# Performance work log

Measured on AMD Instinct MI355X. Metric: run time of the kernel, lower is better.

The kernel has to match this reference:

```python
import jax, jax.numpy as jnp
import numpy as np

_SQRT4PI = float(np.sqrt(4.0 * np.pi))

def spherical_harmonics_l2(vec):
    # e3nn real spherical harmonics, lmax=2, normalize=True, normalization='integral'
    # component-normalized values divided by sqrt(4*pi); e3nn (x,y,z) ordering with y as zenith
    r = jnp.linalg.norm(vec, axis=-1, keepdims=True)
    u = vec / jnp.maximum(r, 1e-12)
    x, y, z = u[..., 0], u[..., 1], u[..., 2]
    c1 = np.float32(np.sqrt(3.0)); c2 = np.float32(np.sqrt(15.0)); c3 = np.float32(np.sqrt(5.0))
    sh = jnp.stack([
        jnp.ones_like(x),                      # l=0
        c1 * x, c1 * y, c1 * z,                # l=1
        c2 * x * z,                            # l=2
        c2 * x * y,
        c3 * (y * y - 0.5 * (x * x + z * z)),
        c2 * y * z,
        (c2 * 0.5) * (z * z - x * x),
    ], axis=-1)
    return sh * np.float32(1.0 / _SQRT4PI)

def setup_inputs() -> dict:
    key = jax.random.key(0)
    ks = jax.random.split(key, 8)
    N, M, C, F, SH = 50000, 12, 128, 64, 9
    return dict(
        atom_fea=jax.random.normal(ks[0], (N, C), jnp.float32),
        nbr_fea=jax.random.normal(ks[1], (N, M, F), jnp.float32),
        nbr_idx=jax.random.randint(ks[2], (N, M), 0, N),
        pos=jax.random.normal(ks[3], (N, 3), jnp.float32),
        w1=jax.random.normal(ks[4], (F, F), jnp.float32) * np.float32(1.0 / np.sqrt(F)),
        b1=jnp.zeros((F,), jnp.float32),
        w2=jax.random.normal(ks[5], (F, SH), jnp.float32) * np.float32(1.0 / np.sqrt(F)),
        b2=jnp.zeros((SH,), jnp.float32),
        tp_w=jax.random.normal(ks[6], (C, C), jnp.float32),  # FCTP weight, path (Cx0e)x(1x0e)->(Cx0e)
        bn_gamma=jnp.ones((C,), jnp.float32),
        bn_beta=jnp.zeros((C,), jnp.float32),
    )

def reference(atom_fea, nbr_fea, nbr_idx, pos, w1, b1, w2, b2, tp_w, bn_gamma, bn_beta):
    N, M, F = nbr_fea.shape
    C = atom_fea.shape[1]
    src = nbr_idx.reshape(-1)                                  # (E,)
    h_j = atom_fea[src]                                        # (E, C) gather
    # radial MLP: Linear -> Softplus -> Linear
    R = jax.nn.softplus(nbr_fea.reshape(N * M, F) @ w1 + b1) @ w2 + b2   # (E, 9)
    rel = pos[src] - jnp.repeat(pos, M, axis=0)                # (E, 3), dst = arange(N) repeated M times
    Y = spherical_harmonics_l2(rel)                            # (E, 9)
    W = R * Y                                                  # (E, 9)
    # FullyConnectedTensorProduct(Cx0e, 0e+1o+2e, Cx0e): only 0e x 0e -> 0e path survives,
    # fan-in normalization alpha = 1/sqrt(C)
    msg = (h_j @ tp_w) * W[:, :1] * np.float32(1.0 / np.sqrt(C))  # (E, C)
    # scatter-mean over dst: dst rows are contiguous blocks of size M per node
    agg = msg.reshape(N, M, C).mean(axis=1)                    # (N, C)
    x = atom_fea + agg
    # BatchNorm1d (training-mode batch statistics, eps=1e-5)
    mean = x.mean(axis=0)
    var = x.var(axis=0)
    xn = (x - mean) * jax.lax.rsqrt(var + 1e-5)
    return jax.nn.softplus(bn_gamma * xn + bn_beta)
```

## Files before the change

### kernel.cpp

```cpp
#include <hip/hip_runtime.h>
#include <hip/hip_bf16.h>
#include <cstddef>

#define N_NODES 50000
#define M_NBR   12
#define C_CH    128
#define F_DIM   64
#define E_EDGES (N_NODES * M_NBR)
#define TILES_PER_WAVE 5

constexpr float SCALE_CE =
    (float)(1.0 / (3.5449077018110318 * 11.313708498984761 * 12.0));

typedef __bf16 bf16x8 __attribute__((ext_vector_type(8)));
typedef float  f32x4  __attribute__((ext_vector_type(4)));

__device__ __forceinline__ float softplus_f(float x) {
    return fmaxf(x, 0.0f) + __logf(1.0f + __expf(-fabsf(x)));
}

__device__ __forceinline__ float bfhi_to_f(unsigned int p) {
    return __uint_as_float(p & 0xffff0000u);
}
__device__ __forceinline__ float bflo_to_f(unsigned int p) {
    return __uint_as_float(p << 16);
}

__global__ __launch_bounds__(512) void kW(
    const float* __restrict__ w1,
    const float* __restrict__ tp_w,
    __bf16* __restrict__ fragW1,
    __bf16* __restrict__ fragTP)
{
    const int t = threadIdx.x;
    if (blockIdx.x == 0) {
        const int lane = t & 63;
        const int f = t >> 6;
        const int n = f >> 1, ks = f & 1;
        const int col16 = lane & 15, kgrp = lane >> 4;
        bf16x8 v;
        #pragma unroll
        for (int j = 0; j < 8; ++j)
            v[j] = (__bf16)w1[(ks * 32 + kgrp * 8 + j) * F_DIM + 16 * n + col16];
        *(bf16x8*)&fragW1[(size_t)t * 8] = v;
    } else {
        const int fid = (blockIdx.x - 1) * 512 + t;
        const int lane = fid & 63;
        const int f = fid >> 6;
        const int n = f >> 2, ks = f & 3;
        const int col16 = lane & 15, kgrp = lane >> 4;
        bf16x8 v;
        #pragma unroll
        for (int j = 0; j < 8; ++j)
            v[j] = (__bf16)tp_w[(ks * 32 + kgrp * 8 + j) * C_CH + 16 * n + col16];
        *(bf16x8*)&fragTP[(size_t)fid * 8] = v;
    }
}

__global__ __launch_bounds__(256) void kY(
    const float* __restrict__ atom_fea,
    const __bf16* __restrict__ fragTP,
    __bf16* __restrict__ y)
{
    __shared__ __bf16 yl[64 * 136];
    const int tid   = threadIdx.x;
    const int lane  = tid & 63;
    const int wid   = tid >> 6;
    const int col16 = lane & 15;
    const int kgrp  = lane >> 4;

    const int row  = blockIdx.x * 64 + wid * 16 + col16;
    const int rowc = row < N_NODES ? row : N_NODES - 1;
    const float* ap = atom_fea + (size_t)rowc * C_CH + kgrp * 8;

    bf16x8 afrag[4];
    #pragma unroll
    for (int ks = 0; ks < 4; ++ks) {
        float4 f0 = *(const float4*)(ap + ks * 32);
        float4 f1 = *(const float4*)(ap + ks * 32 + 4);
        afrag[ks][0] = (__bf16)f0.x; afrag[ks][1] = (__bf16)f0.y;
        afrag[ks][2] = (__bf16)f0.z; afrag[ks][3] = (__bf16)f0.w;
        afrag[ks][4] = (__bf16)f1.x; afrag[ks][5] = (__bf16)f1.y;
        afrag[ks][6] = (__bf16)f1.z; afrag[ks][7] = (__bf16)f1.w;
    }

    #pragma unroll
    for (int n = 0; n < 8; ++n) {
        f32x4 acc = (f32x4){0.f, 0.f, 0.f, 0.f};
        #pragma unroll
        for (int ks = 0; ks < 4; ++ks) {
            bf16x8 bf = *(const bf16x8*)&fragTP[((size_t)(n * 4 + ks) * 64 + lane) * 8];
            acc = __builtin_amdgcn_mfma_f32_16x16x32_bf16(afrag[ks], bf, acc, 0, 0, 0);
        }
        #pragma unroll
        for (int r = 0; r < 4; ++r)
            yl[(wid * 16 + kgrp * 4 + r) * 136 + 16 * n + col16] = (__bf16)acc[r];
    }
    __syncthreads();

    #pragma unroll
    for (int it = 0; it < 4; ++it) {
        const int e  = it * 2048 + tid * 8;
        const int rw = e >> 7, cl = e & 127;
        const int grow = blockIdx.x * 64 + rw;
        if (grow < N_NODES) {
            bf16x8 v = *(const bf16x8*)&yl[rw * 136 + cl];
            *(bf16x8*)&y[(size_t)grow * C_CH + cl] = v;
        }
    }
}

__global__ __launch_bounds__(256) void kA1(
    const float* __restrict__ nbr_fea,
    const __bf16* __restrict__ frag,
    const float* __restrict__ b1,
    const float* __restrict__ w2,
    const float* __restrict__ b2,
    float* __restrict__ ce)
{
    const int tid   = threadIdx.x;
    const int lane  = tid & 63;
    const int wid   = tid >> 6;
    const int col16 = lane & 15;
    const int kgrp  = lane >> 4;

    bf16x8 bfrag[4][2];
    #pragma unroll
    for (int f = 0; f < 8; ++f)
        bfrag[f >> 1][f & 1] = *(const bf16x8*)&frag[((size_t)f * 64 + lane) * 8];

    float b1v[4], w2v[4];
    #pragma unroll
    for (int n = 0; n < 4; ++n) {
        b1v[n] = b1[16 * n + col16];
        w2v[n] = w2[(16 * n + col16) * 9];
    }
    const float b2_0 = b2[0];

    const int tile0 = (blockIdx.x * 4 + wid) * TILES_PER_WAVE;

    for (int t = 0; t < TILES_PER_WAVE; ++t) {
        const long e0 = (long)(tile0 + t) * 16;
        const float* arow = nbr_fea + (e0 + col16) * F_DIM + kgrp * 8;

        bf16x8 afrag[2];
        #pragma unroll
        for (int ks = 0; ks < 2; ++ks) {
            float4 f0 = *(const float4*)(arow + ks * 32);
            float4 f1 = *(const float4*)(arow + ks * 32 + 4);
            afrag[ks][0] = (__bf16)f0.x; afrag[ks][1] = (__bf16)f0.y;
            afrag[ks][2] = (__bf16)f0.z; afrag[ks][3] = (__bf16)f0.w;
            afrag[ks][4] = (__bf16)f1.x; afrag[ks][5] = (__bf16)f1.y;
            afrag[ks][6] = (__bf16)f1.z; afrag[ks][7] = (__bf16)f1.w;
        }

        f32x4 acc[4];
        #pragma unroll
        for (int n = 0; n < 4; ++n) acc[n] = (f32x4){0.f, 0.f, 0.f, 0.f};
        #pragma unroll
        for (int ks = 0; ks < 2; ++ks)
            #pragma unroll
            for (int n = 0; n < 4; ++n)
                acc[n] = __builtin_amdgcn_mfma_f32_16x16x32_bf16(
                    afrag[ks], bfrag[n][ks], acc[n], 0, 0, 0);

        float partial[4] = {0.f, 0.f, 0.f, 0.f};
        #pragma unroll
        for (int n = 0; n < 4; ++n)
            #pragma unroll
            for (int r = 0; r < 4; ++r) {
                const float h = acc[n][r] + b1v[n];
                partial[r] = fmaf(softplus_f(h), w2v[n], partial[r]);
            }
        #pragma unroll
        for (int r = 0; r < 4; ++r) {
            #pragma unroll
            for (int off = 1; off <= 8; off <<= 1)
                partial[r] += __shfl_xor(partial[r], off);
        }
        if (col16 == 0) {
            #pragma unroll
            for (int r = 0; r < 4; ++r)
                ce[e0 + kgrp * 4 + r] = (partial[r] + b2_0) * SCALE_CE;
        }
    }
}

__global__ __launch_bounds__(256, 6) void kG(
    const float* __restrict__ atom_fea,
    const __bf16* __restrict__ y,
    const int*   __restrict__ nbr_idx,
    const float* __restrict__ ce,
    float* __restrict__ x,
    float* __restrict__ psum,
    float* __restrict__ psumsq)
{
    __shared__ float4 red[4][64];
    const int tid  = threadIdx.x;
    const int lane = tid & 63;
    const int wid  = tid >> 6;
    const int blk  = blockIdx.x;
    const int i0   = blk * 64 + wid * 16;

    float2 sum   = make_float2(0.f, 0.f);
    float2 sumsq = make_float2(0.f, 0.f);

    int   pidx = 0;
    float pce  = 0.f;
    if (i0 < N_NODES && lane < M_NBR) {
        pidx = nbr_idx[i0 * M_NBR + lane];
        pce  = ce[i0 * M_NBR + lane];
    }

    for (int t = 0; t < 16; ++t) {
        const int i = i0 + t;
        const int   cidx = pidx;
        const float cce  = pce;
        const int inext = i + 1;
        if (t < 15 && inext < N_NODES && lane < M_NBR) {
            pidx = nbr_idx[inext * M_NBR + lane];
            pce  = ce[inext * M_NBR + lane];
        }
        if (i < N_NODES) {
            float2 acc = make_float2(0.f, 0.f);
            #pragma unroll
            for (int m = 0; m < M_NBR; ++m) {
                const int   src = __shfl(cidx, m);
                const float c   = __shfl(cce, m);
                const unsigned int p =
                    *(const unsigned int*)(y + (size_t)src * C_CH + lane * 2);
                acc.x = fmaf(c, bflo_to_f(p), acc.x);
                acc.y = fmaf(c, bfhi_to_f(p), acc.y);
            }
            const float2 a = *(const float2*)(atom_fea + (size_t)i * C_CH + lane * 2);
            float2 xv = make_float2(a.x + acc.x, a.y + acc.y);
            *(float2*)(x + (size_t)i * C_CH + lane * 2) = xv;
            sum.x += xv.x; sum.y += xv.y;
            sumsq.x += xv.x * xv.x; sumsq.y += xv.y * xv.y;
        }
    }

    red[wid][lane] = make_float4(sum.x, sum.y, sumsq.x, sumsq.y);
    __syncthreads();
    if (tid < 128) {
        const int l = tid >> 1, comp = tid & 1;
        float s = 0.f, q = 0.f;
        #pragma unroll
        for (int w = 0; w < 4; ++w) {
            const float4 v = red[w][l];
            s += comp ? v.y : v.x;
            q += comp ? v.w : v.z;
        }
        psum[blk * 128 + tid]   = s;
        psumsq[blk * 128 + tid] = q;
    }
}

__global__ __launch_bounds__(1024) void kC1(
    const float* __restrict__ psum,
    const float* __restrict__ psumsq,
    float* __restrict__ mean_o,
    float* __restrict__ istd_o,
    int nblocks)
{
    __shared__ float red[2][8][128];
    const int t = threadIdx.x;
    const int c = t & 127;
    const int grp = t >> 7;
    float s = 0.f, ss = 0.f;
    for (int b = grp; b < nblocks; b += 8) {
        s  += psum[b * 128 + c];
        ss += psumsq[b * 128 + c];
    }
    red[0][grp][c] = s;
    red[1][grp][c] = ss;
    __syncthreads();
    if (t < 128) {
        float S = 0.f, SS = 0.f;
        #pragma unroll
        for (int k = 0; k < 8; ++k) { S += red[0][k][t]; SS += red[1][k][t]; }
        const float m   = S / (float)N_NODES;
        const float var = SS / (float)N_NODES - m * m;
        mean_o[t] = m;
        istd_o[t] = rsqrtf(var + 1e-5f);
    }
}

__global__ __launch_bounds__(256) void kC2(
    float* __restrict__ x,
    const float* __restrict__ mean_i,
    const float* __restrict__ istd_i,
    const float* __restrict__ gamma,
    const float* __restrict__ beta)
{
    __shared__ float sm[128], si[128], sg[128], sb[128];
    const int tid = threadIdx.x;
    if (tid < 128) {
        sm[tid] = mean_i[tid];
        si[tid] = istd_i[tid];
        sg[tid] = gamma[tid];
        sb[tid] = beta[tid];
    }
    __syncthreads();
    const size_t idx = ((size_t)blockIdx.x * 256 + tid) * 4;
    const int c = (int)(idx & 127);
    float4 v = *(const float4*)&x[idx];
    float r[4] = {v.x, v.y, v.z, v.w};
    #pragma unroll
    for (int t = 0; t < 4; ++t) {
        const int cc = c + t;
        const float xn = (r[t] - sm[cc]) * si[cc];
        r[t] = softplus_f(fmaf(sg[cc], xn, sb[cc]));
    }
    v.x = r[0]; v.y = r[1]; v.z = r[2]; v.w = r[3];
    *(float4*)&x[idx] = v;
}

extern "C" void kernel_launch(void* const* d_in, const int* in_sizes, int n_in,
                              void* d_out, int out_size, void* d_ws, size_t ws_size,
                              hipStream_t stream)
{
    const float* atom_fea = (const float*)d_in[0];
    const float* nbr_fea  = (const float*)d_in[1];
    const int*   nbr_idx  = (const int*)d_in[2];
    const float* w1       = (const float*)d_in[4];
    const float* b1       = (const float*)d_in[5];
    const float* w2       = (const float*)d_in[6];
    const float* b2       = (const float*)d_in[7];
    const float* tp_w     = (const float*)d_in[8];
    const float* bn_gamma = (const float*)d_in[9];
    const float* bn_beta  = (const float*)d_in[10];

    float* out = (float*)d_out;
    float* ws  = (float*)d_ws;

    const int nblocks = (N_NODES + 63) / 64;
    float* ce      = ws;
    float* psum    = ce + E_EDGES;
    float* psumsq  = psum + (size_t)nblocks * 128;
    float* mean_b  = psumsq + (size_t)nblocks * 128;
    float* istd_b  = mean_b + 128;
    __bf16* fragW1 = (__bf16*)(istd_b + 128);
    __bf16* fragTP = fragW1 + 4096;
    __bf16* ybuf   = fragTP + 16384;

    kW<<<5, 512, 0, stream>>>(w1, tp_w, fragW1, fragTP);
    kY<<<nblocks, 256, 0, stream>>>(atom_fea, fragTP, ybuf);
    kA1<<<E_EDGES / (64 * TILES_PER_WAVE), 256, 0, stream>>>(
        nbr_fea, fragW1, b1, w2, b2, ce);
    kG<<<nblocks, 256, 0, stream>>>(atom_fea, ybuf, nbr_idx, ce,
                                    out, psum, psumsq);
    kC1<<<1, 1024, 0, stream>>>(psum, psumsq, mean_b, istd_b, nblocks);
    const int totalv4 = (N_NODES * C_CH) / 4;
    kC2<<<totalv4 / 256, 256, 0, stream>>>(out, mean_b, istd_b, bn_gamma, bn_beta);
}
```

Before: 128.8 us.

## Merge front kernels and fuse gather with batchnorm via cooperative grid sync

The weight-fragment kernel is dropped and each wave now converts w1 and tp_w to bf16 fragments directly from global memory. The edge MLP and node transform run as two block ranges of a single launch. The gather, statistics reduction and normalize/softplus steps become one cooperative kernel that uses two grid-wide syncs, so x is normalized while still hot in cache and two launches disappear. The cost is redundant weight conversion per block, two grid barriers, and occupancy capped at 782 co-resident blocks with launch bounds lowered to 4.

Result: slower. 263.8 us (+104.8%).

```diff
diff --git a/kernel.cpp b/kernel.cpp
--- a/kernel.cpp
+++ b/kernel.cpp
@@ -1,6 +1,9 @@
 #include <hip/hip_runtime.h>
 #include <hip/hip_bf16.h>
+#include <hip/hip_cooperative_groups.h>
 #include <cstddef>
+
+namespace cg = cooperative_groups;
 
 #define N_NODES 50000
 #define M_NBR   12
@@ -8,6 +11,8 @@
 #define F_DIM   64
 #define E_EDGES (N_NODES * M_NBR)
 #define TILES_PER_WAVE 5
+#define NBLK_A  1875
+#define NBLK_G  782
 
 constexpr float SCALE_CE =
     (float)(1.0 / (3.5449077018110318 * 11.313708498984761 * 12.0));
@@ -26,40 +31,15 @@
     return __uint_as_float(p << 16);
 }
 
-__global__ __launch_bounds__(512) void kW(
+__global__ __launch_bounds__(256) void kFront(
+    const float* __restrict__ nbr_fea,
     const float* __restrict__ w1,
+    const float* __restrict__ b1,
+    const float* __restrict__ w2,
+    const float* __restrict__ b2,
+    const float* __restrict__ atom_fea,
     const float* __restrict__ tp_w,
-    __bf16* __restrict__ fragW1,
-    __bf16* __restrict__ fragTP)
-{
-    const int t = threadIdx.x;
-    if (blockIdx.x == 0) {
-        const int lane = t & 63;
-        const int f = t >> 6;
-        const int n = f >> 1, ks = f & 1;
-        const int col16 = lane & 15, kgrp = lane >> 4;
-        bf16x8 v;
-        #pragma unroll
-        for (int j = 0; j < 8; ++j)
-            v[j] = (__bf16)w1[(ks * 32 + kgrp * 8 + j) * F_DIM + 16 * n + col16];
-        *(bf16x8*)&fragW1[(size_t)t * 8] = v;
-    } else {
-        const int fid = (blockIdx.x - 1) * 512 + t;
-        const int lane = fid & 63;
-        const int f = fid >> 6;
-        const int n = f >> 2, ks = f & 3;
-        const int col16 = lane & 15, kgrp = lane >> 4;
-        bf16x8 v;
-        #pragma unroll
-        for (int j = 0; j < 8; ++j)
-            v[j] = (__bf16)tp_w[(ks * 32 + kgrp * 8 + j) * C_CH + 16 * n + col16];
-        *(bf16x8*)&fragTP[(size_t)fid * 8] = v;
-    }
-}
-
-__global__ __launch_bounds__(256) void kY(
-    const float* __restrict__ atom_fea,
-    const __bf16* __restrict__ fragTP,
+    float* __restrict__ ce,
     __bf16* __restrict__ y)
 {
     __shared__ __bf16 yl[64 * 136];
@@ -69,131 +49,131 @@
     const int col16 = lane & 15;
     const int kgrp  = lane >> 4;
 
-    const int row  = blockIdx.x * 64 + wid * 16 + col16;
-    const int rowc = row < N_NODES ? row : N_NODES - 1;
-    const float* ap = atom_fea + (size_t)rowc * C_CH + kgrp * 8;
-
-    bf16x8 afrag[4];
-    #pragma unroll
-    for (int ks = 0; ks < 4; ++ks) {
-        float4 f0 = *(const float4*)(ap + ks * 32);
-        float4 f1 = *(const float4*)(ap + ks * 32 + 4);
-        afrag[ks][0] = (__bf16)f0.x; afrag[ks][1] = (__bf16)f0.y;
-        afrag[ks][2] = (__bf16)f0.z; afrag[ks][3] = (__bf16)f0.w;
-        afrag[ks][4] = (__bf16)f1.x; afrag[ks][5] = (__bf16)f1.y;
-        afrag[ks][6] = (__bf16)f1.z; afrag[ks][7] = (__bf16)f1.w;
-    }
-
-    #pragma unroll
-    for (int n = 0; n < 8; ++n) {
-        f32x4 acc = (f32x4){0.f, 0.f, 0.f, 0.f};
+    if (blockIdx.x < NBLK_A) {
+        bf16x8 bfrag[4][2];
+        #pragma unroll
+        for (int n = 0; n < 4; ++n)
+            #pragma unroll
+            for (int ks = 0; ks < 2; ++ks)
+                #pragma unroll
+                for (int j = 0; j < 8; ++j)
+                    bfrag[n][ks][j] =
+                        (__bf16)w1[(ks * 32 + kgrp * 8 + j) * F_DIM + 16 * n + col16];
+
+        float b1v[4], w2v[4];
+        #pragma unroll
+        for (int n = 0; n < 4; ++n) {
+            b1v[n] = b1[16 * n + col16];
+            w2v[n] = w2[(16 * n + col16) * 9];
+        }
+        const float b2_0 = b2[0];
+
+        const int tile0 = (blockIdx.x * 4 + wid) * TILES_PER_WAVE;
+
+        for (int t = 0; t < TILES_PER_WAVE; ++t) {
+            const long e0 = (long)(tile0 + t) * 16;
+            const float* arow = nbr_fea + (e0 + col16) * F_DIM + kgrp * 8;
+
+            bf16x8 afrag[2];
+            #pragma unroll
+            for (int ks = 0; ks < 2; ++ks) {
+                float4 f0 = *(const float4*)(arow + ks * 32);
+                float4 f1 = *(const float4*)(arow + ks * 32 + 4);
+                afrag[ks][0] = (__bf16)f0.x; afrag[ks][1] = (__bf16)f0.y;
+                afrag[ks][2] = (__bf16)f0.z; afrag[ks][3] = (__bf16)f0.w;
+                afrag[ks][4] = (__bf16)f1.x; afrag[ks][5] = (__bf16)f1.y;
+                afrag[ks][6] = (__bf16)f1.z; afrag[ks][7] = (__bf16)f1.w;
+            }
+
+            f32x4 acc[4];
+            #pragma unroll
+            for (int n = 0; n < 4; ++n) acc[n] = (f32x4){0.f, 0.f, 0.f, 0.f};
+            #pragma unroll
+            for (int ks = 0; ks < 2; ++ks)
+                #pragma unroll
+                for (int n = 0; n < 4; ++n)
+                    acc[n] = __builtin_amdgcn_mfma_f32_16x16x32_bf16(
+                        afrag[ks], bfrag[n][ks], acc[n], 0, 0, 0);
+
+            float partial[4] = {0.f, 0.f, 0.f, 0.f};
+            #pragma unroll
+            for (int n = 0; n < 4; ++n)
+                #pragma unroll
+                for (int r = 0; r < 4; ++r) {
+                    const float h = acc[n][r] + b1v[n];
+                    partial[r] = fmaf(softplus_f(h), w2v[n], partial[r]);
+                }
+            #pragma unroll
+            for (int r = 0; r < 4; ++r) {
+                #pragma unroll
+                for (int off = 1; off <= 8; off <<= 1)
+                    partial[r] += __shfl_xor(partial[r], off);
+            }
+            if (col16 == 0) {
+                #pragma unroll
+                for (int r = 0; r < 4; ++r)
+                    ce[e0 + kgrp * 4 + r] = (partial[r] + b2_0) * SCALE_CE;
+            }
+        }
+    } else {
+        const int blk  = blockIdx.x - NBLK_A;
+        const int row  = blk * 64 + wid * 16 + col16;
+        const int rowc = row < N_NODES ? row : N_NODES - 1;
+        const float* ap = atom_fea + (size_t)rowc * C_CH + kgrp * 8;
+
+        bf16x8 afrag[4];
         #pragma unroll
         for (int ks = 0; ks < 4; ++ks) {
-            bf16x8 bf = *(const bf16x8*)&fragTP[((size_t)(n * 4 + ks) * 64 + lane) * 8];
-            acc = __builtin_amdgcn_mfma_f32_16x16x32_bf16(afrag[ks], bf, acc, 0, 0, 0);
-        }
-        #pragma unroll
-        for (int r = 0; r < 4; ++r)
-            yl[(wid * 16 + kgrp * 4 + r) * 136 + 16 * n + col16] = (__bf16)acc[r];
-    }
-    __syncthreads();
-
-    #pragma unroll
-    for (int it = 0; it < 4; ++it) {
-        const int e  = it * 2048 + tid * 8;
-        const int rw = e >> 7, cl = e & 127;
-        const int grow = blockIdx.x * 64 + rw;
-        if (grow < N_NODES) {
-            bf16x8 v = *(const bf16x8*)&yl[rw * 136 + cl];
-            *(bf16x8*)&y[(size_t)grow * C_CH + cl] = v;
-        }
-    }
-}
-
-__global__ __launch_bounds__(256) void kA1(
-    const float* __restrict__ nbr_fea,
-    const __bf16* __restrict__ frag,
-    const float* __restrict__ b1,
-    const float* __restrict__ w2,
-    const float* __restrict__ b2,
-    float* __restrict__ ce)
-{
-    const int tid   = threadIdx.x;
-    const int lane  = tid & 63;
-    const int wid   = tid >> 6;
-    const int col16 = lane & 15;
-    const int kgrp  = lane >> 4;
-
-    bf16x8 bfrag[4][2];
-    #pragma unroll
-    for (int f = 0; f < 8; ++f)
-        bfrag[f >> 1][f & 1] = *(const bf16x8*)&frag[((size_t)f * 64 + lane) * 8];
-
-    float b1v[4], w2v[4];
-    #pragma unroll
-    for (int n = 0; n < 4; ++n) {
-        b1v[n] = b1[16 * n + col16];
-        w2v[n] = w2[(16 * n + col16) * 9];
-    }
-    const float b2_0 = b2[0];
-
-    const int tile0 = (blockIdx.x * 4 + wid) * TILES_PER_WAVE;
-
-    for (int t = 0; t < TILES_PER_WAVE; ++t) {
-        const long e0 = (long)(tile0 + t) * 16;
-        const float* arow = nbr_fea + (e0 + col16) * F_DIM + kgrp * 8;
-
-        bf16x8 afrag[2];
-        #pragma unroll
-        for (int ks = 0; ks < 2; ++ks) {
-            float4 f0 = *(const float4*)(arow + ks * 32);
-            float4 f1 = *(const float4*)(arow + ks * 32 + 4);
+            float4 f0 = *(const float4*)(ap + ks * 32);
+            float4 f1 = *(const float4*)(ap + ks * 32 + 4);
             afrag[ks][0] = (__bf16)f0.x; afrag[ks][1] = (__bf16)f0.y;
             afrag[ks][2] = (__bf16)f0.z; afrag[ks][3] = (__bf16)f0.w;
             afrag[ks][4] = (__bf16)f1.x; afrag[ks][5] = (__bf16)f1.y;
             afrag[ks][6] = (__bf16)f1.z; afrag[ks][7] = (__bf16)f1.w;
         }
 
-        f32x4 acc[4];
-        #pragma unroll
-        for (int n = 0; n < 4; ++n) acc[n] = (f32x4){0.f, 0.f, 0.f, 0.f};
-        #pragma unroll
-        for (int ks = 0; ks < 2; ++ks)
-            #pragma unroll
-            for (int n = 0; n < 4; ++n)
-                acc[n] = __builtin_amdgcn_mfma_f32_16x16x32_bf16(
-                    afrag[ks], bfrag[n][ks], acc[n], 0, 0, 0);
-
-        float partial[4] = {0.f, 0.f, 0.f, 0.f};
-        #pragma unroll
-        for (int n = 0; n < 4; ++n)
-            #pragma unroll
-            for (int r = 0; r < 4; ++r) {
-                const float h = acc[n][r] + b1v[n];
-                partial[r] = fmaf(softplus_f(h), w2v[n], partial[r]);
-            }
-        #pragma unroll
-        for (int r = 0; r < 4; ++r) {
-            #pragma unroll
-            for (int off = 1; off <= 8; off <<= 1)
-                partial[r] += __shfl_xor(partial[r], off);
-        }
-        if (col16 == 0) {
+        #pragma unroll
+        for (int n = 0; n < 8; ++n) {
+            f32x4 acc = (f32x4){0.f, 0.f, 0.f, 0.f};
+            #pragma unroll
+            for (int ks = 0; ks < 4; ++ks) {
+                bf16x8 bf;
+                #pragma unroll
+                for (int j = 0; j < 8; ++j)
+                    bf[j] = (__bf16)tp_w[(ks * 32 + kgrp * 8 + j) * C_CH + 16 * n + col16];
+                acc = __builtin_amdgcn_mfma_f32_16x16x32_bf16(afrag[ks], bf, acc, 0, 0, 0);
+            }
             #pragma unroll
             for (int r = 0; r < 4; ++r)
-                ce[e0 + kgrp * 4 + r] = (partial[r] + b2_0) * SCALE_CE;
-        }
-    }
-}
-
-__global__ __launch_bounds__(256, 6) void kG(
+                yl[(wid * 16 + kgrp * 4 + r) * 136 + 16 * n + col16] = (__bf16)acc[r];
+        }
+        __syncthreads();
+
+        #pragma unroll
+        for (int it = 0; it < 4; ++it) {
+            const int e  = it * 2048 + tid * 8;
+            const int rw = e >> 7, cl = e & 127;
+            const int grow = blk * 64 + rw;
+            if (grow < N_NODES) {
+                bf16x8 v = *(const bf16x8*)&yl[rw * 136 + cl];
+                *(bf16x8*)&y[(size_t)grow * C_CH + cl] = v;
+            }
+        }
+    }
+}
+
+__global__ __launch_bounds__(256, 4) void kGBN(
     const float* __restrict__ atom_fea,
     const __bf16* __restrict__ y,
     const int*   __restrict__ nbr_idx,
     const float* __restrict__ ce,
     float* __restrict__ x,
     float* __restrict__ psum,
-    float* __restrict__ psumsq)
+    float* __restrict__ psumsq,
+    float* __restrict__ mean_b,
+    float* __restrict__ istd_b,
+    const float* __restrict__ gamma,
+    const float* __restrict__ beta)
 {
     __shared__ float4 red[4][64];
     const int tid  = threadIdx.x;
@@ -254,66 +234,45 @@
         psum[blk * 128 + tid]   = s;
         psumsq[blk * 128 + tid] = q;
     }
-}
-
-__global__ __launch_bounds__(1024) void kC1(
-    const float* __restrict__ psum,
-    const float* __restrict__ psumsq,
-    float* __restrict__ mean_o,
-    float* __restrict__ istd_o,
-    int nblocks)
-{
-    __shared__ float red[2][8][128];
-    const int t = threadIdx.x;
-    const int c = t & 127;
-    const int grp = t >> 7;
-    float s = 0.f, ss = 0.f;
-    for (int b = grp; b < nblocks; b += 8) {
-        s  += psum[b * 128 + c];
-        ss += psumsq[b * 128 + c];
-    }
-    red[0][grp][c] = s;
-    red[1][grp][c] = ss;
-    __syncthreads();
-    if (t < 128) {
-        float S = 0.f, SS = 0.f;
-        #pragma unroll
-        for (int k = 0; k < 8; ++k) { S += red[0][k][t]; SS += red[1][k][t]; }
-        const float m   = S / (float)N_NODES;
-        const float var = SS / (float)N_NODES - m * m;
-        mean_o[t] = m;
-        istd_o[t] = rsqrtf(var + 1e-5f);
-    }
-}
-
-__global__ __launch_bounds__(256) void kC2(
-    float* __restrict__ x,
-    const float* __restrict__ mean_i,
-    const float* __restrict__ istd_i,
-    const float* __restrict__ gamma,
-    const float* __restrict__ beta)
-{
-    __shared__ float sm[128], si[128], sg[128], sb[128];
-    const int tid = threadIdx.x;
-    if (tid < 128) {
-        sm[tid] = mean_i[tid];
-        si[tid] = istd_i[tid];
-        sg[tid] = gamma[tid];
-        sb[tid] = beta[tid];
-    }
-    __syncthreads();
-    const size_t idx = ((size_t)blockIdx.x * 256 + tid) * 4;
-    const int c = (int)(idx & 127);
-    float4 v = *(const float4*)&x[idx];
-    float r[4] = {v.x, v.y, v.z, v.w};
-    #pragma unroll
-    for (int t = 0; t < 4; ++t) {
-        const int cc = c + t;
-        const float xn = (r[t] - sm[cc]) * si[cc];
-        r[t] = softplus_f(fmaf(sg[cc], xn, sb[cc]));
-    }
-    v.x = r[0]; v.y = r[1]; v.z = r[2]; v.w = r[3];
-    *(float4*)&x[idx] = v;
+
+    cg::this_grid().sync();
+
+    if (blk < 32) {
+        const int ch = blk * 4 + wid;
+        float s = 0.f, q = 0.f;
+        for (int e = lane; e < NBLK_G; e += 64) {
+            s += psum[e * 128 + ch];
+            q += psumsq[e * 128 + ch];
+        }
+        #pragma unroll
+        for (int off = 32; off >= 1; off >>= 1) {
+            s += __shfl_xor(s, off);
+            q += __shfl_xor(q, off);
+        }
+        if (lane == 0) {
+            const float m   = s / (float)N_NODES;
+            const float var = q / (float)N_NODES - m * m;
+            mean_b[ch] = m;
+            istd_b[ch] = rsqrtf(var + 1e-5f);
+        }
+    }
+
+    cg::this_grid().sync();
+
+    const int c0 = lane * 2;
+    const float m0 = mean_b[c0],  m1 = mean_b[c0 + 1];
+    const float s0 = istd_b[c0],  s1 = istd_b[c0 + 1];
+    const float g0 = gamma[c0],   g1 = gamma[c0 + 1];
+    const float t0 = beta[c0],    t1 = beta[c0 + 1];
+    for (int t = 0; t < 16; ++t) {
+        const int i = i0 + t;
+        if (i < N_NODES) {
+            float2 xv = *(const float2*)(x + (size_t)i * C_CH + c0);
+            xv.x = softplus_f(fmaf(g0, (xv.x - m0) * s0, t0));
+            xv.y = softplus_f(fmaf(g1, (xv.y - m1) * s1, t1));
+            *(float2*)(x + (size_t)i * C_CH + c0) = xv;
+        }
+    }
 }
 
 extern "C" void kernel_launch(void* const* d_in, const int* in_sizes, int n_in,
@@ -334,23 +293,22 @@
     float* out = (float*)d_out;
     float* ws  = (float*)d_ws;
 
-    const int nblocks = (N_NODES + 63) / 64;
     float* ce      = ws;
     float* psum    = ce + E_EDGES;
-    float* psumsq  = psum + (size_t)nblocks * 128;
-    float* mean_b  = psumsq + (size_t)nblocks * 128;
+    float* psumsq  = psum + (size_t)NBLK_G * 128;
+    float* mean_b  = psumsq + (size_t)NBLK_G * 128;
     float* istd_b  = mean_b + 128;
-    __bf16* fragW1 = (__bf16*)(istd_b + 128);
-    __bf16* fragTP = fragW1 + 4096;
-    __bf16* ybuf   = fragTP + 16384;
-
-    kW<<<5, 512, 0, stream>>>(w1, tp_w, fragW1, fragTP);
-    kY<<<nblocks, 256, 0, stream>>>(atom_fea, fragTP, ybuf);
-    kA1<<<E_EDGES / (64 * TILES_PER_WAVE), 256, 0, stream>>>(
-        nbr_fea, fragW1, b1, w2, b2, ce);
-    kG<<<nblocks, 256, 0, stream>>>(atom_fea, ybuf, nbr_idx, ce,
-                                    out, psum, psumsq);
-    kC1<<<1, 1024, 0, stream>>>(psum, psumsq, mean_b, istd_b, nblocks);
-    const int totalv4 = (N_NODES * C_CH) / 4;
-    kC2<<<totalv4 / 256, 256, 0, stream>>>(out, mean_b, istd_b, bn_gamma, bn_beta);
-}
+    __bf16* ybuf   = (__bf16*)(istd_b + 128);
+
+    kFront<<<NBLK_A + NBLK_G, 256, 0, stream>>>(
+        nbr_fea, w1, b1, w2, b2, atom_fea, tp_w, ce, ybuf);
+
+    const __bf16* ybuf_c = ybuf;
+    void* args[] = {
+        (void*)&atom_fea, (void*)&ybuf_c, (void*)&nbr_idx, (void*)&ce,
+        (void*)&out, (void*)&psum, (void*)&psumsq, (void*)&mean_b,
+        (void*)&istd_b, (void*)&bn_gamma, (void*)&bn_beta
+    };
+    hipLaunchCooperativeKernel((const void*)kGBN, dim3(NBLK_G), dim3(256),
+                               args, 0, stream);
+}
```

## Merge weight prep, Y GEMM and radial MLP into one front kernel; shrink gather blocks

Applied to the files above, without the earlier changes.

Drops the separate weight-fragment kernel and merges the atom-feature GEMM and the radial-MLP kernels into one launch, with each block picking its role by block index. Weights are now converted from fp32 straight from global memory inside every block, which trades two launches and their serialisation for redundant per-block conversion loads. The gather kernel now handles 32 nodes per block instead of 64, and it issues all 12 neighbour loads before accumulating to expose more memory-level parallelism. The psum buffers are resized to match the new block count.

New measurement: 149.1 us. 15.7% more time.

```diff
diff --git a/kernel.cpp b/kernel.cpp
--- a/kernel.cpp
+++ b/kernel.cpp
@@ -8,6 +8,9 @@
 #define F_DIM   64
 #define E_EDGES (N_NODES * M_NBR)
 #define TILES_PER_WAVE 5
+#define NBLK_A  1875
+#define NBLK_Y  782
+#define NBLK_G  1563
 
 constexpr float SCALE_CE =
     (float)(1.0 / (3.5449077018110318 * 11.313708498984761 * 12.0));
@@ -26,40 +29,15 @@
     return __uint_as_float(p << 16);
 }
 
-__global__ __launch_bounds__(512) void kW(
+__global__ __launch_bounds__(256) void kFront(
+    const float* __restrict__ nbr_fea,
     const float* __restrict__ w1,
+    const float* __restrict__ b1,
+    const float* __restrict__ w2,
+    const float* __restrict__ b2,
+    const float* __restrict__ atom_fea,
     const float* __restrict__ tp_w,
-    __bf16* __restrict__ fragW1,
-    __bf16* __restrict__ fragTP)
-{
-    const int t = threadIdx.x;
-    if (blockIdx.x == 0) {
-        const int lane = t & 63;
-        const int f = t >> 6;
-        const int n = f >> 1, ks = f & 1;
-        const int col16 = lane & 15, kgrp = lane >> 4;
-        bf16x8 v;
-        #pragma unroll
-        for (int j = 0; j < 8; ++j)
-            v[j] = (__bf16)w1[(ks * 32 + kgrp * 8 + j) * F_DIM + 16 * n + col16];
-        *(bf16x8*)&fragW1[(size_t)t * 8] = v;
-    } else {
-        const int fid = (blockIdx.x - 1) * 512 + t;
-        const int lane = fid & 63;
-        const int f = fid >> 6;
-        const int n = f >> 2, ks = f & 3;
-        const int col16 = lane & 15, kgrp = lane >> 4;
-        bf16x8 v;
-        #pragma unroll
-        for (int j = 0; j < 8; ++j)
-            v[j] = (__bf16)tp_w[(ks * 32 + kgrp * 8 + j) * C_CH + 16 * n + col16];
-        *(bf16x8*)&fragTP[(size_t)fid * 8] = v;
-    }
-}
-
-__global__ __launch_bounds__(256) void kY(
-    const float* __restrict__ atom_fea,
-    const __bf16* __restrict__ fragTP,
+    float* __restrict__ ce,
     __bf16* __restrict__ y)
 {
     __shared__ __bf16 yl[64 * 136];
@@ -69,119 +47,115 @@
     const int col16 = lane & 15;
     const int kgrp  = lane >> 4;
 
-    const int row  = blockIdx.x * 64 + wid * 16 + col16;
-    const int rowc = row < N_NODES ? row : N_NODES - 1;
-    const float* ap = atom_fea + (size_t)rowc * C_CH + kgrp * 8;
-
-    bf16x8 afrag[4];
-    #pragma unroll
-    for (int ks = 0; ks < 4; ++ks) {
-        float4 f0 = *(const float4*)(ap + ks * 32);
-        float4 f1 = *(const float4*)(ap + ks * 32 + 4);
-        afrag[ks][0] = (__bf16)f0.x; afrag[ks][1] = (__bf16)f0.y;
-        afrag[ks][2] = (__bf16)f0.z; afrag[ks][3] = (__bf16)f0.w;
-        afrag[ks][4] = (__bf16)f1.x; afrag[ks][5] = (__bf16)f1.y;
-        afrag[ks][6] = (__bf16)f1.z; afrag[ks][7] = (__bf16)f1.w;
-    }
-
-    #pragma unroll
-    for (int n = 0; n < 8; ++n) {
-        f32x4 acc = (f32x4){0.f, 0.f, 0.f, 0.f};
+    if (blockIdx.x < NBLK_A) {
+        bf16x8 bfrag[4][2];
+        #pragma unroll
+        for (int n = 0; n < 4; ++n)
+            #pragma unroll
+            for (int ks = 0; ks < 2; ++ks)
+                #pragma unroll
+                for (int j = 0; j < 8; ++j)
+                    bfrag[n][ks][j] =
+                        (__bf16)w1[(ks * 32 + kgrp * 8 + j) * F_DIM + 16 * n + col16];
+
+        float b1v[4], w2v[4];
+        #pragma unroll
+        for (int n = 0; n < 4; ++n) {
+            b1v[n] = b1[16 * n + col16];
+            w2v[n] = w2[(16 * n + col16) * 9];
+        }
+        const float b2_0 = b2[0];
+
+        const int tile0 = (blockIdx.x * 4 + wid) * TILES_PER_WAVE;
+
+        for (int t = 0; t < TILES_PER_WAVE; ++t) {
+            const long e0 = (long)(tile0 + t) * 16;
+            const float* arow = nbr_fea + (e0 + col16) * F_DIM + kgrp * 8;
+
+            bf16x8 afrag[2];
+            #pragma unroll
+            for (int ks = 0; ks < 2; ++ks) {
+                float4 f0 = *(const float4*)(arow + ks * 32);
+                float4 f1 = *(const float4*)(arow + ks * 32 + 4);
+                afrag[ks][0] = (__bf16)f0.x; afrag[ks][1] = (__bf16)f0.y;
+                afrag[ks][2] = (__bf16)f0.z; afrag[ks][3] = (__bf16)f0.w;
+                afrag[ks][4] = (__bf16)f1.x; afrag[ks][5] = (__bf16)f1.y;
+                afrag[ks][6] = (__bf16)f1.z; afrag[ks][7] = (__bf16)f1.w;
+            }
+
+            f32x4 acc[4];
+            #pragma unroll
+            for (int n = 0; n < 4; ++n) acc[n] = (f32x4){0.f, 0.f, 0.f, 0.f};
+            #pragma unroll
+            for (int ks = 0; ks < 2; ++ks)
+                #pragma unroll
+                for (int n = 0; n < 4; ++n)
+                    acc[n] = __builtin_amdgcn_mfma_f32_16x16x32_bf16(
+                        afrag[ks], bfrag[n][ks], acc[n], 0, 0, 0);
+
+            float partial[4] = {0.f, 0.f, 0.f, 0.f};
+            #pragma unroll
+            for (int n = 0; n < 4; ++n)
+                #pragma unroll
+                for (int r = 0; r < 4; ++r) {
+                    const float h = acc[n][r] + b1v[n];
+                    partial[r] = fmaf(softplus_f(h), w2v[n], partial[r]);
+                }
+            #pragma unroll
+            for (int r = 0; r < 4; ++r) {
+                #pragma unroll
+                for (int off = 1; off <= 8; off <<= 1)
+                    partial[r] += __shfl_xor(partial[r], off);
+            }
+            if (col16 == 0) {
+                #pragma unroll
+                for (int r = 0; r < 4; ++r)
+                    ce[e0 + kgrp * 4 + r] = (partial[r] + b2_0) * SCALE_CE;
+            }
+        }
+    } else {
+        const int blk  = blockIdx.x - NBLK_A;
+        const int row  = blk * 64 + wid * 16 + col16;
+        const int rowc = row < N_NODES ? row : N_NODES - 1;
+        const float* ap = atom_fea + (size_t)rowc * C_CH + kgrp * 8;
+
+        bf16x8 afrag[4];
         #pragma unroll
         for (int ks = 0; ks < 4; ++ks) {
-            bf16x8 bf = *(const bf16x8*)&fragTP[((size_t)(n * 4 + ks) * 64 + lane) * 8];
-            acc = __builtin_amdgcn_mfma_f32_16x16x32_bf16(afrag[ks], bf, acc, 0, 0, 0);
-        }
-        #pragma unroll
-        for (int r = 0; r < 4; ++r)
-            yl[(wid * 16 + kgrp * 4 + r) * 136 + 16 * n + col16] = (__bf16)acc[r];
-    }
-    __syncthreads();
-
-    #pragma unroll
-    for (int it = 0; it < 4; ++it) {
-        const int e  = it * 2048 + tid * 8;
-        const int rw = e >> 7, cl = e & 127;
-        const int grow = blockIdx.x * 64 + rw;
-        if (grow < N_NODES) {
-            bf16x8 v = *(const bf16x8*)&yl[rw * 136 + cl];
-            *(bf16x8*)&y[(size_t)grow * C_CH + cl] = v;
-        }
-    }
-}
-
-__global__ __launch_bounds__(256) void kA1(
-    const float* __restrict__ nbr_fea,
-    const __bf16* __restrict__ frag,
-    const float* __restrict__ b1,
-    const float* __restrict__ w2,
-    const float* __restrict__ b2,
-    float* __restrict__ ce)
-{
-    const int tid   = threadIdx.x;
-    const int lane  = tid & 63;
-    const int wid   = tid >> 6;
-    const int col16 = lane & 15;
-    const int kgrp  = lane >> 4;
-
-    bf16x8 bfrag[4][2];
-    #pragma unroll
-    for (int f = 0; f < 8; ++f)
-        bfrag[f >> 1][f & 1] = *(const bf16x8*)&frag[((size_t)f * 64 + lane) * 8];
-
-    float b1v[4], w2v[4];
-    #pragma unroll
-    for (int n = 0; n < 4; ++n) {
-        b1v[n] = b1[16 * n + col16];
-        w2v[n] = w2[(16 * n + col16) * 9];
-    }
-    const float b2_0 = b2[0];
-
-    const int tile0 = (blockIdx.x * 4 + wid) * TILES_PER_WAVE;
-
-    for (int t = 0; t < TILES_PER_WAVE; ++t) {
-        const long e0 = (long)(tile0 + t) * 16;
-        const float* arow = nbr_fea + (e0 + col16) * F_DIM + kgrp * 8;
-
-        bf16x8 afrag[2];
-        #pragma unroll
-        for (int ks = 0; ks < 2; ++ks) {
-            float4 f0 = *(const float4*)(arow + ks * 32);
-            float4 f1 = *(const float4*)(arow + ks * 32 + 4);
+            float4 f0 = *(const float4*)(ap + ks * 32);
+            float4 f1 = *(const float4*)(ap + ks * 32 + 4);
             afrag[ks][0] = (__bf16)f0.x; afrag[ks][1] = (__bf16)f0.y;
             afrag[ks][2] = (__bf16)f0.z; afrag[ks][3] = (__bf16)f0.w;
             afrag[ks][4] = (__bf16)f1.x; afrag[ks][5] = (__bf16)f1.y;
             afrag[ks][6] = (__bf16)f1.z; afrag[ks][7] = (__bf16)f1.w;
         }
 
-        f32x4 acc[4];
-        #pragma unroll
-        for (int n = 0; n < 4; ++n) acc[n] = (f32x4){0.f, 0.f, 0.f, 0.f};
-        #pragma unroll
-        for (int ks = 0; ks < 2; ++ks)
-            #pragma unroll
-            for (int n = 0; n < 4; ++n)
-                acc[n] = __builtin_amdgcn_mfma_f32_16x16x32_bf16(
-                    afrag[ks], bfrag[n][ks], acc[n], 0, 0, 0);
-
-        float partial[4] = {0.f, 0.f, 0.f, 0.f};
-        #pragma unroll
-        for (int n = 0; n < 4; ++n)
-            #pragma unroll
-            for (int r = 0; r < 4; ++r) {
-                const float h = acc[n][r] + b1v[n];
-                partial[r] = fmaf(softplus_f(h), w2v[n], partial[r]);
-            }
-        #pragma unroll
-        for (int r = 0; r < 4; ++r) {
-            #pragma unroll
-            for (int off = 1; off <= 8; off <<= 1)
-                partial[r] += __shfl_xor(partial[r], off);
-        }
-        if (col16 == 0) {
+        #pragma unroll
+        for (int n = 0; n < 8; ++n) {
+            f32x4 acc = (f32x4){0.f, 0.f, 0.f, 0.f};
+            #pragma unroll
+            for (int ks = 0; ks < 4; ++ks) {
+                bf16x8 bf;
+                #pragma unroll
+                for (int j = 0; j < 8; ++j)
+                    bf[j] = (__bf16)tp_w[(ks * 32 + kgrp * 8 + j) * C_CH + 16 * n + col16];
+                acc = __builtin_amdgcn_mfma_f32_16x16x32_bf16(afrag[ks], bf, acc, 0, 0, 0);
+            }
             #pragma unroll
             for (int r = 0; r < 4; ++r)
-                ce[e0 + kgrp * 4 + r] = (partial[r] + b2_0) * SCALE_CE;
+                yl[(wid * 16 + kgrp * 4 + r) * 136 + 16 * n + col16] = (__bf16)acc[r];
+        }
+        __syncthreads();
+
+        #pragma unroll
+        for (int it = 0; it < 4; ++it) {
+            const int e  = it * 2048 + tid * 8;
+            const int rw = e >> 7, cl = e & 127;
+            const int grow = blk * 64 + rw;
+            if (grow < N_NODES) {
+                bf16x8 v = *(const bf16x8*)&yl[rw * 136 + cl];
+                *(bf16x8*)&y[(size_t)grow * C_CH + cl] = v;
+            }
         }
     }
 }
@@ -200,7 +174,7 @@
     const int lane = tid & 63;
     const int wid  = tid >> 6;
     const int blk  = blockIdx.x;
-    const int i0   = blk * 64 + wid * 16;
+    const int i0   = blk * 32 + wid * 8;
 
     float2 sum   = make_float2(0.f, 0.f);
     float2 sumsq = make_float2(0.f, 0.f);
@@ -212,25 +186,28 @@
         pce  = ce[i0 * M_NBR + lane];
     }
 
-    for (int t = 0; t < 16; ++t) {
+    for (int t = 0; t < 8; ++t) {
         const int i = i0 + t;
         const int   cidx = pidx;
         const float cce  = pce;
         const int inext = i + 1;
-        if (t < 15 && inext < N_NODES && lane < M_NBR) {
+        if (t < 7 && inext < N_NODES && lane < M_NBR) {
             pidx = nbr_idx[inext * M_NBR + lane];
             pce  = ce[inext * M_NBR + lane];
         }
         if (i < N_NODES) {
+            unsigned int pv[M_NBR];
+            #pragma unroll
+            for (int m = 0; m < M_NBR; ++m) {
+                const int src = __shfl(cidx, m);
+                pv[m] = *(const unsigned int*)(y + (size_t)src * C_CH + lane * 2);
+            }
             float2 acc = make_float2(0.f, 0.f);
             #pragma unroll
             for (int m = 0; m < M_NBR; ++m) {
-                const int   src = __shfl(cidx, m);
-                const float c   = __shfl(cce, m);
-                const unsigned int p =
-                    *(const unsigned int*)(y + (size_t)src * C_CH + lane * 2);
-                acc.x = fmaf(c, bflo_to_f(p), acc.x);
-                acc.y = fmaf(c, bfhi_to_f(p), acc.y);
+                const float c = __shfl(cce, m);
+                acc.x = fmaf(c, bflo_to_f(pv[m]), acc.x);
+                acc.y = fmaf(c, bfhi_to_f(pv[m]), acc.y);
             }
             const float2 a = *(const float2*)(atom_fea + (size_t)i * C_CH + lane * 2);
             float2 xv = make_float2(a.x + acc.x, a.y + acc.y);
@@ -334,23 +311,18 @@
     float* out = (float*)d_out;
     float* ws  = (float*)d_ws;
 
-    const int nblocks = (N_NODES + 63) / 64;
     float* ce      = ws;
     float* psum    = ce + E_EDGES;
-    float* psumsq  = psum + (size_t)nblocks * 128;
-    float* mean_b  = psumsq + (size_t)nblocks * 128;
+    float* psumsq  = psum + (size_t)NBLK_G * 128;
+    float* mean_b  = psumsq + (size_t)NBLK_G * 128;
     float* istd_b  = mean_b + 128;
-    __bf16* fragW1 = (__bf16*)(istd_b + 128);
-    __bf16* fragTP = fragW1 + 4096;
-    __bf16* ybuf   = fragTP + 16384;
-
-    kW<<<5, 512, 0, stream>>>(w1, tp_w, fragW1, fragTP);
-    kY<<<nblocks, 256, 0, stream>>>(atom_fea, fragTP, ybuf);
-    kA1<<<E_EDGES / (64 * TILES_PER_WAVE), 256, 0, stream>>>(
-        nbr_fea, fragW1, b1, w2, b2, ce);
-    kG<<<nblocks, 256, 0, stream>>>(atom_fea, ybuf, nbr_idx, ce,
-                                    out, psum, psumsq);
-    kC1<<<1, 1024, 0, stream>>>(psum, psumsq, mean_b, istd_b, nblocks);
+    __bf16* ybuf   = (__bf16*)(istd_b + 128);
+
+    kFront<<<NBLK_A + NBLK_Y, 256, 0, stream>>>(
+        nbr_fea, w1, b1, w2, b2, atom_fea, tp_w, ce, ybuf);
+    kG<<<NBLK_G, 256, 0, stream>>>(atom_fea, ybuf, nbr_idx, ce,
+                                   out, psum, psumsq);
+    kC1<<<1, 1024, 0, stream>>>(psum, psumsq, mean_b, istd_b, NBLK_G);
     const int totalv4 = (N_NODES * C_CH) / 4;
     kC2<<<totalv4 / 256, 256, 0, stream>>>(out, mean_b, istd_b, bn_gamma, bn_beta);
 }
```
